# Kernel optimization log

Measured on AMD Instinct MI355X. Metric: run time of the kernel, lower is better.

The kernel has to match this reference:

```python
import jax, jax.numpy as jnp
import numpy as np

N_EMBED = 2048
N_HEAD = 2
HEAD_SIZE = N_EMBED // N_HEAD  # 1024; mask constraint requires T <= HEAD_SIZE


def setup_inputs() -> dict:
    key = jax.random.key(0)
    ks = jax.random.split(key, 9)
    B, T, C, H, D = 32, 1024, N_EMBED, N_HEAD, HEAD_SIZE
    s = 1.0 / np.sqrt(C)
    x = jax.random.normal(ks[0], (B, T, C), dtype=jnp.float32)
    # torch Linear convention: weight (out_features, in_features), y = x @ W.T + b
    Wq = jax.random.normal(ks[1], (H, D, C), dtype=jnp.float32) * s
    Wk = jax.random.normal(ks[2], (H, D, C), dtype=jnp.float32) * s
    Wv = jax.random.normal(ks[3], (H, D, C), dtype=jnp.float32) * s
    bq = jax.random.normal(ks[4], (H, D), dtype=jnp.float32) * 0.01
    bk = jax.random.normal(ks[5], (H, D), dtype=jnp.float32) * 0.01
    bv = jax.random.normal(ks[6], (H, D), dtype=jnp.float32) * 0.01
    Wo = jax.random.normal(ks[7], (C, H * D), dtype=jnp.float32) * s  # no bias
    return {"x": x, "Wq": Wq, "bq": bq, "Wk": Wk, "bk": bk, "Wv": Wv, "bv": bv, "Wo": Wo}


def reference(x, Wq, bq, Wk, bk, Wv, bv, Wo):
    B, T, C = x.shape
    # per-head projections, batched over heads: (B,T,C) x (H,D,C) -> (B,H,T,D)
    q = jnp.einsum('btc,hdc->bhtd', x, Wq) + bq[None, :, None, :]
    k = jnp.einsum('btc,hdc->bhtd', x, Wk) + bk[None, :, None, :]
    v = jnp.einsum('btc,hdc->bhtd', x, Wv) + bv[None, :, None, :]
    # NOTE: original scales by x.shape[-1]**-0.5 == n_embed**-0.5 (not head_size)
    scale = jnp.asarray(C, x.dtype) ** -0.5
    wei = jnp.einsum('bhtd,bhsd->bhts', q, k) * scale  # (B,H,T,T)
    causal = jnp.tril(jnp.ones((T, T), dtype=bool))
    wei = jnp.where(causal[None, None], wei, -jnp.inf)
    wei = jax.nn.softmax(wei, axis=-1)
    out = jnp.einsum('bhts,bhsd->bhtd', wei, v)  # (B,H,T,D)
    # concat heads along last dim: (B,T,H*D)
    out = out.transpose(0, 2, 1, 3).reshape(B, T, -1)
    return out @ Wo.T  # (B,T,C)
```

## Files before the change

### kernel.cpp

```cpp
#include <hip/hip_runtime.h>
#include <hip/hip_bf16.h>
#include <stdint.h>

typedef __bf16 bf16_t;
typedef __bf16 bf16x8 __attribute__((ext_vector_type(8)));
typedef float f32x4 __attribute__((ext_vector_type(4)));

#define AS1(p) ((const __attribute__((address_space(1))) void*)(uintptr_t)(p))
#define AS3(p) ((__attribute__((address_space(3))) void*)(uintptr_t)(p))

__device__ __forceinline__ void gload16(const bf16_t* g, bf16_t* l) {
  __builtin_amdgcn_global_load_lds(AS1(g), AS3(l), 16, 0, 0);
}

#define SB()      __builtin_amdgcn_sched_barrier(0);
#define BAR()     { __builtin_amdgcn_sched_barrier(0); __builtin_amdgcn_s_barrier(); __builtin_amdgcn_sched_barrier(0); }
#define VMCNT(n)  { asm volatile("s_waitcnt vmcnt(" #n ")" ::: "memory"); __builtin_amdgcn_sched_barrier(0); }
#define LGKM(n)   { asm volatile("s_waitcnt lgkmcnt(" #n ")" ::: "memory"); __builtin_amdgcn_sched_barrier(0); }

__device__ __forceinline__ void gemm256(const bf16_t* __restrict__ A, int lda,
                                        const bf16_t* __restrict__ B, int ldb,
                                        int nt, f32x4 acc[8][4], bf16_t* lds) {
  const int t = (int)threadIdx.x;
  const int lane = t & 63, w = t >> 6;
  const int wr = w >> 2, wc = w & 3;
  const int fr = lane & 15, fq = lane >> 4;
  char* ldsb = (char*)lds;

  const int s0 = (t * 16) ^ (((t >> 3) & 7) << 4);
  const int r0 = s0 >> 6, q0 = (s0 >> 4) & 3;
  const bf16_t* gA0 = A + (size_t)r0 * lda + q0 * 8;
  const bf16_t* gA1 = gA0 + (size_t)128 * lda;
  const bf16_t* gB0 = B + (size_t)r0 * ldb + q0 * 8;
  const bf16_t* gB1 = gB0 + (size_t)128 * ldb;

  const int swz = (fr * 64 + fq * 16) ^ (((fr >> 1) & 7) << 4);
  const int abase = wr * 8192 + swz;
  const int bbase = 32768 + wc * 4096 + swz;

  bf16x8 bb[4], aa0[4], aa1[4];

#define STAGE_A(cb, kh, kof) { \
    bf16_t* _d = lds + (cb) * 32768 + (kh) * 8192; \
    gload16(gA0 + (kof) + (kh) * 32, _d + t * 8); \
    gload16(gA1 + (kof) + (kh) * 32, _d + 4096 + t * 8); \
  } SB()
#define STAGE_B(cb, kh, kof) { \
    bf16_t* _d = lds + (cb) * 32768 + 16384 + (kh) * 8192; \
    gload16(gB0 + (kof) + (kh) * 32, _d + t * 8); \
    gload16(gB1 + (kof) + (kh) * 32, _d + 4096 + t * 8); \
  } SB()
#define READ_B(cb, kh) { \
    const char* _b = ldsb + (cb) * 65536 + (kh) * 16384 + bbase; \
    _Pragma("unroll") for (int n = 0; n < 4; ++n) bb[n] = *(const bf16x8*)(_b + n * 1024); }
#define READ_A(cb, kh, qm, dst) { \
    const char* _a = ldsb + (cb) * 65536 + (kh) * 16384 + abase + (qm) * 4096; \
    _Pragma("unroll") for (int i = 0; i < 4; ++i) dst[i] = *(const bf16x8*)(_a + i * 1024); }
#define MFMA16(dst, qm) { \
    __builtin_amdgcn_s_setprio(1); \
    _Pragma("unroll") for (int i = 0; i < 4; ++i) \
      _Pragma("unroll") for (int n = 0; n < 4; ++n) \
        acc[(qm) * 4 + i][n] = __builtin_amdgcn_mfma_f32_16x16x32_bf16(dst[i], bb[n], acc[(qm) * 4 + i][n], 0, 0, 0); \
    __builtin_amdgcn_s_setprio(0); }

  STAGE_A(0, 0, 0) STAGE_B(0, 0, 0) STAGE_A(0, 1, 0) STAGE_B(0, 1, 0)

  int kof = 64;
  for (int tt = 0; tt < nt - 1; ++tt, kof += 64) {
    const int cb = tt & 1;
    VMCNT(4) BAR()
    READ_B(cb, 0) READ_A(cb, 0, 0, aa0)
    STAGE_A(cb ^ 1, 0, kof)
    READ_A(cb, 0, 1, aa1)
    STAGE_B(cb ^ 1, 0, kof)
    LGKM(4) MFMA16(aa0, 0)
    LGKM(0) MFMA16(aa1, 1)
    VMCNT(4) BAR()
    READ_B(cb, 1) READ_A(cb, 1, 0, aa0)
    STAGE_A(cb ^ 1, 1, kof)
    READ_A(cb, 1, 1, aa1)
    STAGE_B(cb ^ 1, 1, kof)
    LGKM(4) MFMA16(aa0, 0)
    LGKM(0) MFMA16(aa1, 1)
  }
  {
    const int cb = (nt - 1) & 1;
    VMCNT(4) BAR()
    READ_B(cb, 0) READ_A(cb, 0, 0, aa0) READ_A(cb, 0, 1, aa1)
    LGKM(4) MFMA16(aa0, 0)
    LGKM(0) MFMA16(aa1, 1)
    VMCNT(0) BAR()
    READ_B(cb, 1) READ_A(cb, 1, 0, aa0) READ_A(cb, 1, 1, aa1)
    LGKM(4) MFMA16(aa0, 0)
    LGKM(0) MFMA16(aa1, 1)
  }
#undef STAGE_A
#undef STAGE_B
#undef READ_B
#undef READ_A
#undef MFMA16
}

#define EPI_VARS \
  const int t = (int)threadIdx.x; \
  const int lane = t & 63, w = t >> 6; \
  const int wr = w >> 2, wc = w & 3; \
  const int fr = lane & 15, fq = lane >> 4;

#define ZERO8x4(acc) \
  _Pragma("unroll") for (int _i = 0; _i < 8; ++_i) \
  _Pragma("unroll") for (int _j = 0; _j < 4; ++_j) { f32x4 _z = {0.f,0.f,0.f,0.f}; acc[_i][_j] = _z; }

__global__ void k_cvt(const float* __restrict__ s, bf16_t* __restrict__ d, long n8) {
  long i = (long)blockIdx.x * blockDim.x + threadIdx.x;
  long st = (long)gridDim.x * blockDim.x;
  for (; i < n8; i += st) {
    const float4* sp = (const float4*)(s + i * 8);
    float4 a = sp[0], b = sp[1];
    bf16x8 v;
    v[0] = (__bf16)a.x; v[1] = (__bf16)a.y; v[2] = (__bf16)a.z; v[3] = (__bf16)a.w;
    v[4] = (__bf16)b.x; v[5] = (__bf16)b.y; v[6] = (__bf16)b.z; v[7] = (__bf16)b.w;
    *(bf16x8*)(d + i * 8) = v;
  }
}

__global__ void k_fill(float* o, float v, long n) {
  long i = (long)blockIdx.x * blockDim.x + threadIdx.x;
  long st = (long)gridDim.x * blockDim.x;
  for (; i < n; i += st) o[i] = v;
}

__global__ __launch_bounds__(512, 2) void k_qkv256(
    const bf16_t* __restrict__ xb, const bf16_t* __restrict__ Wb,
    const float* __restrict__ bq, const float* __restrict__ bk, const float* __restrict__ bv,
    bf16_t* __restrict__ Q, bf16_t* __restrict__ K, bf16_t* __restrict__ Vt) {
  __shared__ __align__(16) bf16_t lds[65536];
  int bid = (int)blockIdx.x;
  int id = (bid & 7) * 384 + (bid >> 3);
  EPI_VARS
  f32x4 acc[8][4];
  ZERO8x4(acc)

  bool vmode = id >= 2048;
  int mt = 0, ntile = 0, tok = 0, wm = 0;
  const bf16_t *Ap, *Bp;
  if (!vmode) {
    mt = id & 127; ntile = id >> 7;
    Ap = xb + (size_t)mt * 256 * 2048;
    Bp = Wb + (size_t)ntile * 256 * 2048;
  } else {
    int vb = id - 2048;
    tok = vb & 127; wm = vb >> 7;
    Ap = Wb + (size_t)(16 + wm) * 256 * 2048;
    Bp = xb + (size_t)tok * 256 * 2048;
  }
  gemm256(Ap, 2048, Bp, 2048, 32, acc, lds);

  if (!vmode) {
    int sel = ntile >> 3;
    const float* bias = sel ? bk : bq;
    bf16_t* dst = sel ? K : Q;
    int cbase = (ntile & 7) * 256 + wc * 64;
#pragma unroll
    for (int ni = 0; ni < 4; ++ni) {
      int c2 = cbase + ni * 16 + fr;
      int h = c2 >> 10, d = c2 & 1023;
      float bb = bias[c2];
#pragma unroll
      for (int mi = 0; mi < 8; ++mi) {
        f32x4 a = acc[mi][ni];
#pragma unroll
        for (int r = 0; r < 4; ++r) {
          int m = mt * 256 + wr * 128 + mi * 16 + fq * 4 + r;
          int b = m >> 10, tk = m & 1023;
          dst[(((size_t)(b * 2 + h) << 10) + tk) * 1024 + d] = (bf16_t)(a[r] + bb);
        }
      }
    }
  } else {
#pragma unroll
    for (int mi = 0; mi < 8; ++mi) {
#pragma unroll
      for (int r = 0; r < 4; ++r) {
        int gd = wm * 256 + wr * 128 + mi * 16 + fq * 4 + r;
        int h = gd >> 10, dd = gd & 1023;
        float bb = bv[gd];
#pragma unroll
        for (int ni = 0; ni < 4; ++ni) {
          int m = tok * 256 + wc * 64 + ni * 16 + fr;
          int b = m >> 10, tk = m & 1023;
          Vt[(((size_t)(b * 2 + h) << 10) + dd) * 1024 + tk] = (bf16_t)(acc[mi][ni][r] + bb);
        }
      }
    }
  }
}

__global__ __launch_bounds__(512, 2) void k_s256(const bf16_t* __restrict__ Q,
                                                 const bf16_t* __restrict__ K,
                                                 bf16_t* __restrict__ S, int pbase) {
  __shared__ __align__(16) bf16_t lds[65536];
  int id = (int)blockIdx.x;
  int pc = id / 10, rem = id % 10;
  int ti = 0;
  while (rem > ti) { rem -= ti + 1; ++ti; }
  int tj = rem;
  size_t p = (size_t)(pbase + pc);
  EPI_VARS
  f32x4 acc[8][4];
  ZERO8x4(acc)
  gemm256(Q + (p << 20) + (size_t)ti * 256 * 1024, 1024,
          K + (p << 20) + (size_t)tj * 256 * 1024, 1024, 16, acc, lds);
  bf16_t* Sp = S + ((size_t)pc << 20);
  const float scale = 0.022097086912079608f;
#pragma unroll
  for (int mi = 0; mi < 8; ++mi)
#pragma unroll
    for (int ni = 0; ni < 4; ++ni) {
      int col = tj * 256 + wc * 64 + ni * 16 + fr;
      f32x4 a = acc[mi][ni];
#pragma unroll
      for (int r = 0; r < 4; ++r) {
        int row = ti * 256 + wr * 128 + mi * 16 + fq * 4 + r;
        Sp[((size_t)row << 10) + col] = (bf16_t)(a[r] * scale);
      }
    }
}

__global__ __launch_bounds__(256) void k_softmax(const bf16_t* __restrict__ S,
                                                 bf16_t* __restrict__ P) {
  int gw = (int)blockIdx.x * 4 + ((int)threadIdx.x >> 6);
  int pc = gw >> 10, row = gw & 1023;
  int lane = (int)threadIdx.x & 63;
  const bf16_t* s = S + ((size_t)pc << 20) + ((size_t)row << 10);
  bf16_t* p = P + ((size_t)pc << 20) + ((size_t)row << 10);
  int cend = ((row >> 8) + 1) << 8;
  bf16x8 v0 = *(const bf16x8*)(s + lane * 8);
  bf16x8 v1 = *(const bf16x8*)(s + 512 + lane * 8);
  float x[16];
  float mx = -1e30f;
#pragma unroll
  for (int j = 0; j < 8; ++j) {
    int c0 = lane * 8 + j, c1 = 512 + lane * 8 + j;
    x[j]     = (c0 <= row) ? (float)v0[j] : -1e30f;
    x[8 + j] = (c1 <= row) ? (float)v1[j] : -1e30f;
    mx = fmaxf(mx, fmaxf(x[j], x[8 + j]));
  }
  for (int o = 32; o > 0; o >>= 1) mx = fmaxf(mx, __shfl_xor(mx, o));
  float sum = 0.f;
#pragma unroll
  for (int j = 0; j < 16; ++j) {
    x[j] = (x[j] > -1e29f) ? __expf(x[j] - mx) : 0.f;
    sum += x[j];
  }
  for (int o = 32; o > 0; o >>= 1) sum += __shfl_xor(sum, o);
  float inv = 1.f / sum;
  bf16x8 o0, o1;
#pragma unroll
  for (int j = 0; j < 8; ++j) {
    o0[j] = (bf16_t)(x[j] * inv);
    o1[j] = (bf16_t)(x[8 + j] * inv);
  }
  if (lane * 8 < cend)       *(bf16x8*)(p + lane * 8) = o0;
  if (512 + lane * 8 < cend) *(bf16x8*)(p + 512 + lane * 8) = o1;
}

__global__ __launch_bounds__(512, 2) void k_pv256(const bf16_t* __restrict__ P,
                                                  const bf16_t* __restrict__ Vt,
                                                  bf16_t* __restrict__ O, int pbase) {
  __shared__ __align__(16) bf16_t lds[65536];
  int id = (int)blockIdx.x;
  int pc = id >> 4, rem = id & 15;
  int ti = rem >> 2, dj = rem & 3;
  size_t p = (size_t)(pbase + pc);
  EPI_VARS
  f32x4 acc[8][4];
  ZERO8x4(acc)
  gemm256(P + ((size_t)pc << 20) + (size_t)ti * 256 * 1024, 1024,
          Vt + (p << 20) + (size_t)dj * 256 * 1024, 1024, (ti + 1) * 4, acc, lds);
  int b = (int)(p >> 1), h = (int)(p & 1);
#pragma unroll
  for (int mi = 0; mi < 8; ++mi)
#pragma unroll
    for (int ni = 0; ni < 4; ++ni) {
      int dcol = dj * 256 + wc * 64 + ni * 16 + fr;
      f32x4 a = acc[mi][ni];
#pragma unroll
      for (int r = 0; r < 4; ++r) {
        int tk = ti * 256 + wr * 128 + mi * 16 + fq * 4 + r;
        O[(((size_t)b << 10) + tk) * 2048 + (h << 10) + dcol] = (bf16_t)a[r];
      }
    }
}

__global__ __launch_bounds__(512, 2) void k_out256(const bf16_t* __restrict__ O,
                                                   const bf16_t* __restrict__ W,
                                                   float* __restrict__ out) {
  __shared__ __align__(16) bf16_t lds[65536];
  int bid = (int)blockIdx.x;
  int id = (bid & 7) * 128 + (bid >> 3);
  int mt = id & 127, ntile = id >> 7;
  EPI_VARS
  f32x4 acc[8][4];
  ZERO8x4(acc)
  gemm256(O + (size_t)mt * 256 * 2048, 2048, W + (size_t)ntile * 256 * 2048, 2048, 32, acc, lds);
#pragma unroll
  for (int mi = 0; mi < 8; ++mi)
#pragma unroll
    for (int ni = 0; ni < 4; ++ni) {
      int col = ntile * 256 + wc * 64 + ni * 16 + fr;
      f32x4 a = acc[mi][ni];
#pragma unroll
      for (int r = 0; r < 4; ++r) {
        int row = mt * 256 + wr * 128 + mi * 16 + fq * 4 + r;
        out[(size_t)row * 2048 + col] = a[r];
      }
    }
}

extern "C" void kernel_launch(void* const* d_in, const int* in_sizes, int n_in,
                              void* d_out, int out_size, void* d_ws, size_t ws_size,
                              hipStream_t stream) {
  const float* x  = (const float*)d_in[0];
  const float* Wq = (const float*)d_in[1];
  const float* bq = (const float*)d_in[2];
  const float* Wk = (const float*)d_in[3];
  const float* bk = (const float*)d_in[4];
  const float* Wv = (const float*)d_in[5];
  const float* bv = (const float*)d_in[6];
  const float* Wo = (const float*)d_in[7];
  float* out = (float*)d_out;

  const size_t MiB = 1ull << 20;
  char* w = (char*)d_ws;
  bf16_t* xb    = (bf16_t*)w;
  bf16_t* Ob    = xb;
  bf16_t* Qb    = (bf16_t*)(w + 128 * MiB);
  bf16_t* Kb    = (bf16_t*)(w + 256 * MiB);
  bf16_t* Vt    = (bf16_t*)(w + 384 * MiB);
  bf16_t* Wqkvb = (bf16_t*)(w + 512 * MiB);
  bf16_t* Wob   = (bf16_t*)(w + 536 * MiB);
  bf16_t* Sc    = (bf16_t*)(w + 544 * MiB);

  size_t rem = ws_size > 544 * MiB ? ws_size - 544 * MiB : 0;
  int NP = (int)(rem / (4 * MiB));
  if (NP > 64) NP = 64;
  if (NP < 1) {
    k_fill<<<2048, 256, 0, stream>>>(out, (float)(ws_size >> 20), (long)out_size);
    return;
  }
  bf16_t* Pc = (bf16_t*)(w + 544 * MiB + (size_t)NP * 2 * MiB);

  k_cvt<<<2048, 256, 0, stream>>>(x, xb, 8388608L);
  k_cvt<<<1024, 256, 0, stream>>>(Wq, Wqkvb, 524288L);
  k_cvt<<<1024, 256, 0, stream>>>(Wk, Wqkvb + 4194304, 524288L);
  k_cvt<<<1024, 256, 0, stream>>>(Wv, Wqkvb + 8388608, 524288L);
  k_cvt<<<1024, 256, 0, stream>>>(Wo, Wob, 524288L);

  k_qkv256<<<3072, 512, 0, stream>>>(xb, Wqkvb, bq, bk, bv, Qb, Kb, Vt);

  for (int base = 0; base < 64; base += NP) {
    int np = (64 - base) < NP ? (64 - base) : NP;
    k_s256<<<np * 10, 512, 0, stream>>>(Qb, Kb, Sc, base);
    k_softmax<<<np * 256, 256, 0, stream>>>(Sc, Pc);
    k_pv256<<<np * 16, 512, 0, stream>>>(Pc, Vt, Ob, base);
  }

  k_out256<<<1024, 512, 0, stream>>>(Ob, Wob, out);
}
```

Measured before the change: 1.475 ms.

## Merge weight conversions, run softmax in place, and drop leading sched barrier

Replaces the four weight conversion launches with a single kernel that selects the source by index range and writes into contiguous bf16 weight storage (Wqkvb followed by Wob). Softmax now writes probabilities back into the score buffer, removing the separate P buffer. This halves workspace per chunk, so NP can double and fewer attention chunk iterations are needed. The GEMM barrier macro also drops the sched_barrier before s_barrier, loosening instruction scheduling. In-place softmax is only safe if each row is fully read before it is written.

```diff
diff --git a/kernel.cpp b/kernel.cpp
--- a/kernel.cpp
+++ b/kernel.cpp
@@ -14,7 +14,7 @@
 }
 
 #define SB()      __builtin_amdgcn_sched_barrier(0);
-#define BAR()     { __builtin_amdgcn_sched_barrier(0); __builtin_amdgcn_s_barrier(); __builtin_amdgcn_sched_barrier(0); }
+#define BARR()    { __builtin_amdgcn_s_barrier(); __builtin_amdgcn_sched_barrier(0); }
 #define VMCNT(n)  { asm volatile("s_waitcnt vmcnt(" #n ")" ::: "memory"); __builtin_amdgcn_sched_barrier(0); }
 #define LGKM(n)   { asm volatile("s_waitcnt lgkmcnt(" #n ")" ::: "memory"); __builtin_amdgcn_sched_barrier(0); }
 
@@ -22,8 +22,8 @@
                                         const bf16_t* __restrict__ B, int ldb,
                                         int nt, f32x4 acc[8][4], bf16_t* lds) {
   const int t = (int)threadIdx.x;
-  const int lane = t & 63, w = t >> 6;
-  const int wr = w >> 2, wc = w & 3;
+  const int lane = t & 63, wv = t >> 6;
+  const int wr = wv >> 2, wc = wv & 3;
   const int fr = lane & 15, fq = lane >> 4;
   char* ldsb = (char*)lds;
 
@@ -68,14 +68,14 @@
   int kof = 64;
   for (int tt = 0; tt < nt - 1; ++tt, kof += 64) {
     const int cb = tt & 1;
-    VMCNT(4) BAR()
+    VMCNT(4) BARR()
     READ_B(cb, 0) READ_A(cb, 0, 0, aa0)
     STAGE_A(cb ^ 1, 0, kof)
     READ_A(cb, 0, 1, aa1)
     STAGE_B(cb ^ 1, 0, kof)
     LGKM(4) MFMA16(aa0, 0)
     LGKM(0) MFMA16(aa1, 1)
-    VMCNT(4) BAR()
+    VMCNT(4) BARR()
     READ_B(cb, 1) READ_A(cb, 1, 0, aa0)
     STAGE_A(cb ^ 1, 1, kof)
     READ_A(cb, 1, 1, aa1)
@@ -85,11 +85,11 @@
   }
   {
     const int cb = (nt - 1) & 1;
-    VMCNT(4) BAR()
+    VMCNT(4) BARR()
     READ_B(cb, 0) READ_A(cb, 0, 0, aa0) READ_A(cb, 0, 1, aa1)
     LGKM(4) MFMA16(aa0, 0)
     LGKM(0) MFMA16(aa1, 1)
-    VMCNT(0) BAR()
+    VMCNT(0) BARR()
     READ_B(cb, 1) READ_A(cb, 1, 0, aa0) READ_A(cb, 1, 1, aa1)
     LGKM(4) MFMA16(aa0, 0)
     LGKM(0) MFMA16(aa1, 1)
@@ -117,6 +117,22 @@
   for (; i < n8; i += st) {
     const float4* sp = (const float4*)(s + i * 8);
     float4 a = sp[0], b = sp[1];
+    bf16x8 v;
+    v[0] = (__bf16)a.x; v[1] = (__bf16)a.y; v[2] = (__bf16)a.z; v[3] = (__bf16)a.w;
+    v[4] = (__bf16)b.x; v[5] = (__bf16)b.y; v[6] = (__bf16)b.z; v[7] = (__bf16)b.w;
+    *(bf16x8*)(d + i * 8) = v;
+  }
+}
+
+__global__ void k_cvtw(const float* __restrict__ Wq, const float* __restrict__ Wk,
+                       const float* __restrict__ Wv, const float* __restrict__ Wo,
+                       bf16_t* __restrict__ d) {
+  long i = (long)blockIdx.x * blockDim.x + threadIdx.x;
+  long st = (long)gridDim.x * blockDim.x;
+  for (; i < 2097152L; i += st) {
+    int r = (int)(i >> 19);
+    const float* s = (r == 0 ? Wq : r == 1 ? Wk : r == 2 ? Wv : Wo) + (i & 524287L) * 8;
+    float4 a = ((const float4*)s)[0], b = ((const float4*)s)[1];
     bf16x8 v;
     v[0] = (__bf16)a.x; v[1] = (__bf16)a.y; v[2] = (__bf16)a.z; v[3] = (__bf16)a.w;
     v[4] = (__bf16)b.x; v[5] = (__bf16)b.y; v[6] = (__bf16)b.z; v[7] = (__bf16)b.w;
@@ -343,27 +359,23 @@
   bf16_t* Sc    = (bf16_t*)(w + 544 * MiB);
 
   size_t rem = ws_size > 544 * MiB ? ws_size - 544 * MiB : 0;
-  int NP = (int)(rem / (4 * MiB));
+  int NP = (int)(rem / (2 * MiB));
   if (NP > 64) NP = 64;
   if (NP < 1) {
     k_fill<<<2048, 256, 0, stream>>>(out, (float)(ws_size >> 20), (long)out_size);
     return;
   }
-  bf16_t* Pc = (bf16_t*)(w + 544 * MiB + (size_t)NP * 2 * MiB);
 
   k_cvt<<<2048, 256, 0, stream>>>(x, xb, 8388608L);
-  k_cvt<<<1024, 256, 0, stream>>>(Wq, Wqkvb, 524288L);
-  k_cvt<<<1024, 256, 0, stream>>>(Wk, Wqkvb + 4194304, 524288L);
-  k_cvt<<<1024, 256, 0, stream>>>(Wv, Wqkvb + 8388608, 524288L);
-  k_cvt<<<1024, 256, 0, stream>>>(Wo, Wob, 524288L);
+  k_cvtw<<<2048, 256, 0, stream>>>(Wq, Wk, Wv, Wo, Wqkvb);
 
   k_qkv256<<<3072, 512, 0, stream>>>(xb, Wqkvb, bq, bk, bv, Qb, Kb, Vt);
 
   for (int base = 0; base < 64; base += NP) {
     int np = (64 - base) < NP ? (64 - base) : NP;
     k_s256<<<np * 10, 512, 0, stream>>>(Qb, Kb, Sc, base);
-    k_softmax<<<np * 256, 256, 0, stream>>>(Sc, Pc);
-    k_pv256<<<np * 16, 512, 0, stream>>>(Pc, Vt, Ob, base);
+    k_softmax<<<np * 256, 256, 0, stream>>>(Sc, Sc);
+    k_pv256<<<np * 16, 512, 0, stream>>>(Sc, Vt, Ob, base);
   }
 
   k_out256<<<1024, 512, 0, stream>>>(Ob, Wob, out);
```

Result: no change. 1.475 ms (-0.0%).
